# Optimization experiments

Measured on AMD Instinct MI355X. Metric: run time of the kernel, lower is better.

## Reference

```python
import jax, jax.numpy as jnp
import numpy as np

LN_EPS = 1e-5

def setup_inputs() -> dict:
    key = jax.random.key(0)
    k1, k2, k3 = jax.random.split(key, 3)
    L, B, D = 2048, 8, 1024
    x = jax.random.normal(k1, (L, B, D), dtype=jnp.float32)
    c = jnp.zeros((B, D), dtype=jnp.float32)
    W = jax.random.normal(k2, (D, 3 * D), dtype=jnp.float32) * 0.02
    # bias init from _init_bias: u-bias 0, f-bias 0.5, r-bias 0
    b = jnp.concatenate([jnp.zeros(D), jnp.full((D,), 0.5), jnp.zeros(D)]).astype(jnp.float32)
    gamma = jnp.ones((D,), dtype=jnp.float32)
    beta = jnp.zeros((D,), dtype=jnp.float32)
    return {"x": x, "c": c, "W": W, "b": b, "gamma": gamma, "beta": beta}

def reference(x, c, W, b, gamma, beta):
    # LayerNorm over last dim
    mu = jnp.mean(x, axis=-1, keepdims=True)
    var = jnp.mean(jnp.square(x - mu), axis=-1, keepdims=True)
    x_norm = (x - mu) * jax.lax.rsqrt(var + LN_EPS) * gamma + beta
    # Fused u/f/r projection: [L,B,3D]
    ufr = jnp.einsum('lbd,de->lbe', x_norm, W) + b
    u, f, r = jnp.split(ufr, 3, axis=-1)
    f_gate = jax.nn.sigmoid(f)
    r_gate = jax.nn.sigmoid(r)
    # Linear recurrence c_t = f_t * c_{t-1} + (1-f_t) * u_t via scan over time
    def step(c_prev, fu):
        f_t, u_t = fu
        c_t = f_t * c_prev + (1.0 - f_t) * u_t
        return c_t, c_t
    last_c, c_stack = jax.lax.scan(step, c, (f_gate, u))
    hs = r_gate * jnp.tanh(c_stack) + (1.0 - r_gate) * x_norm
    return x + hs, last_c
```

## Files before the change

kernel.cpp:

```cpp
#include <hip/hip_runtime.h>
#include <hip/hip_bf16.h>


typedef unsigned short u16;
typedef __bf16 bf16x8 __attribute__((ext_vector_type(8)));
typedef float f32x4 __attribute__((ext_vector_type(4)));

#define L_DIM 2048
#define B_DIM 8
#define D_DIM 1024
#define M_DIM (L_DIM * B_DIM)
#define K_DIM D_DIM
#define N_DIM (3 * D_DIM)
#define NCH 32
#define CLEN (L_DIM / NCH)
#define NT (K_DIM / 64)

#define LDS_A 0
#define LDS_B 65536
#define LDS_DUMMY 131072
#define LDS_TOTAL 147456

__device__ __forceinline__ float bf2f(u16 h) {
    unsigned int u = ((unsigned int)h) << 16;
    float f;
    __builtin_memcpy(&f, &u, 4);
    return f;
}

__device__ __forceinline__ u16 f2bf(float f) {
    unsigned int u;
    __builtin_memcpy(&u, &f, 4);
    u = u + 0x7fff + ((u >> 16) & 1);
    return (u16)(u >> 16);
}

__device__ __forceinline__ void async16(void* lds, const void* g) {
    __builtin_amdgcn_global_load_lds(
        (const __attribute__((address_space(1))) void*)g,
        (__attribute__((address_space(3))) void*)lds, 16, 0, 0);
}

__global__ __launch_bounds__(256) void ln_kernel(const float* __restrict__ x,
                                                 const float* __restrict__ gamma,
                                                 const float* __restrict__ beta,
                                                 u16* __restrict__ xn) {
    int row = blockIdx.x;
    int tid = threadIdx.x;
    const float4* xr = (const float4*)(x + (size_t)row * D_DIM);
    float4 v = xr[tid];
    float s = v.x + v.y + v.z + v.w;
    float q = v.x * v.x + v.y * v.y + v.z * v.z + v.w * v.w;
    #pragma unroll
    for (int off = 32; off; off >>= 1) {
        s += __shfl_down(s, off);
        q += __shfl_down(q, off);
    }
    __shared__ float ss[4], qq[4];
    int lane = tid & 63, wv = tid >> 6;
    if (lane == 0) { ss[wv] = s; qq[wv] = q; }
    __syncthreads();
    s = ss[0] + ss[1] + ss[2] + ss[3];
    q = qq[0] + qq[1] + qq[2] + qq[3];
    float mu = s * (1.0f / D_DIM);
    float var = q * (1.0f / D_DIM) - mu * mu;
    float rs = rsqrtf(var + 1e-5f);
    float4 g = ((const float4*)gamma)[tid];
    float4 bt = ((const float4*)beta)[tid];
    ushort4 o;
    o.x = f2bf((v.x - mu) * rs * g.x + bt.x);
    o.y = f2bf((v.y - mu) * rs * g.y + bt.y);
    o.z = f2bf((v.z - mu) * rs * g.z + bt.z);
    o.w = f2bf((v.w - mu) * rs * g.w + bt.w);
    ((ushort4*)(xn + (size_t)row * D_DIM))[tid] = o;
}

__global__ __launch_bounds__(256) void wt_kernel(const float* __restrict__ W,
                                                 u16* __restrict__ Wt) {
    __shared__ float t[64][65];
    int k0 = blockIdx.x * 64;
    int n0 = blockIdx.y * 64;
    int col = threadIdx.x & 63;
    int rg4 = threadIdx.x >> 6;
    #pragma unroll
    for (int j = 0; j < 16; ++j) {
        int r = rg4 * 16 + j;
        t[r][col] = W[(size_t)(k0 + r) * N_DIM + n0 + col];
    }
    __syncthreads();
    #pragma unroll
    for (int j = 0; j < 16; ++j) {
        int nr = rg4 * 16 + j;
        Wt[(size_t)(n0 + nr) * K_DIM + k0 + col] = f2bf(t[col][nr]);
    }
}

__device__ __forceinline__ void stage_half(const u16* __restrict__ gsrc, int base0,
                                           int t, int h, char* lds, int ldsOp,
                                           int tid, int wave) {
    int tc = (t < NT) ? t : 0;
    int k0 = tc * 64;
    char* dst0 = (t < NT) ? (lds + ldsOp + (t & 1) * 32768 + h * 16384)
                          : (lds + LDS_DUMMY);
    #pragma unroll
    for (int s = 0; s < 2; ++s) {
        int c = s * 512 + tid;
        int row = h * 128 + (c >> 3);
        int cc = (c & 7) ^ (row & 7);
        async16(dst0 + s * 8192 + wave * 1024,
                gsrc + (size_t)(base0 + row) * K_DIM + k0 + cc * 8);
    }
}

__global__ __launch_bounds__(512, 2) void gemm_kernel(const u16* __restrict__ A,
                                                      const u16* __restrict__ Bt,
                                                      const float* __restrict__ bias,
                                                      u16* __restrict__ uo,
                                                      u16* __restrict__ fo,
                                                      u16* __restrict__ ro) {
    extern __shared__ char lds[];
    const int tid = threadIdx.x;
    const int wave = tid >> 6, lane = tid & 63;
    const int lm = lane & 15, lg = lane >> 4;
    const int wm = wave >> 2, wn = wave & 3;
    const int m0 = blockIdx.x * 256;
    const int n0 = blockIdx.y * 256;

    f32x4 acc[8][4] = {};
    bf16x8 av[4][2], aw[4][2], bv[4][2];

#define LDA(dst, bb, mf0)                                                       \
    do { _Pragma("unroll")                                                      \
        for (int q = 0; q < 4; ++q) {                                           \
            int row_ = wm * 128 + ((mf0) + q) * 16 + lm;                        \
            const char* p_ = lds + LDS_A + (bb) * 32768 + row_ * 128;           \
            _Pragma("unroll")                                                   \
            for (int kk = 0; kk < 2; ++kk)                                      \
                dst[q][kk] = *(const bf16x8*)(p_ + ((((kk << 2) | lg) ^ (row_ & 7)) << 4)); \
        } } while (0)

#define LDB(bb, kk)                                                             \
    do { _Pragma("unroll")                                                      \
        for (int nf = 0; nf < 4; ++nf) {                                        \
            int row_ = wn * 64 + nf * 16 + lm;                                  \
            bv[nf][kk] = *(const bf16x8*)(lds + LDS_B + (bb) * 32768 + row_ * 128 \
                                          + ((((kk << 2) | lg) ^ (row_ & 7)) << 4)); \
        } } while (0)

#define MFMA16(r0, afr, kk)                                                     \
    do { _Pragma("unroll")                                                      \
        for (int q = 0; q < 4; ++q)                                             \
            _Pragma("unroll")                                                   \
            for (int nf = 0; nf < 4; ++nf)                                      \
                acc[(r0) + q][nf] = __builtin_amdgcn_mfma_f32_16x16x32_bf16(    \
                    afr[q][kk], bv[nf][kk], acc[(r0) + q][nf], 0, 0, 0);        \
    } while (0)

#define PH_SYNC()                                                               \
    do { __builtin_amdgcn_s_barrier();                                          \
         asm volatile("s_waitcnt lgkmcnt(0)");                                  \
         __builtin_amdgcn_sched_barrier(0); } while (0)

#define TILE_BODY(t, bb, last)                                                  \
    do {                                                                        \
                 \
        LDA(av, bb, 0);                                                         \
        LDB(bb, 0);                                                             \
        stage_half(A, m0, (t) + 1, 0, lds, LDS_A, tid, wave);                   \
        PH_SYNC();                                                              \
        __builtin_amdgcn_s_setprio(1);                                          \
        MFMA16(0, av, 0);                                                       \
        __builtin_amdgcn_s_setprio(0);                                          \
        __builtin_amdgcn_s_barrier();                                           \
                                     \
        LDB(bb, 1);                                                             \
        stage_half(A, m0, (t) + 1, 1, lds, LDS_A, tid, wave);                   \
        PH_SYNC();                                                              \
        __builtin_amdgcn_s_setprio(1);                                          \
        MFMA16(0, av, 1);                                                       \
        __builtin_amdgcn_s_setprio(0);                                          \
        __builtin_amdgcn_s_barrier();                                           \
                                   \
        LDA(aw, bb, 4);                                                         \
        stage_half(Bt, n0, (t) + 2, 0, lds, LDS_B, tid, wave);                  \
        PH_SYNC();                                                              \
        __builtin_amdgcn_s_setprio(1);                                          \
        MFMA16(4, aw, 0);                                                       \
        __builtin_amdgcn_s_setprio(0);                                          \
        __builtin_amdgcn_s_barrier();                                           \
                         \
        stage_half(Bt, n0, (t) + 2, 1, lds, LDS_B, tid, wave);                  \
        __builtin_amdgcn_s_barrier();                                           \
        __builtin_amdgcn_s_setprio(1);                                          \
        MFMA16(4, aw, 1);                                                       \
        __builtin_amdgcn_s_setprio(0);                                          \
        if (!(last)) asm volatile("s_waitcnt vmcnt(4)" ::: "memory");           \
        __builtin_amdgcn_s_barrier();                                           \
    } while (0)

    stage_half(A, m0, 0, 0, lds, LDS_A, tid, wave);
    stage_half(A, m0, 0, 1, lds, LDS_A, tid, wave);
    stage_half(Bt, n0, 0, 0, lds, LDS_B, tid, wave);
    stage_half(Bt, n0, 0, 1, lds, LDS_B, tid, wave);
    stage_half(Bt, n0, 1, 0, lds, LDS_B, tid, wave);
    stage_half(Bt, n0, 1, 1, lds, LDS_B, tid, wave);
    asm volatile("s_waitcnt vmcnt(4)" ::: "memory");
    __builtin_amdgcn_s_barrier();

    for (int t = 0; t < NT - 2; t += 2) {
        TILE_BODY(t, 0, 0);
        TILE_BODY(t + 1, 1, 0);
    }
    TILE_BODY(NT - 2, 0, 0);
    TILE_BODY(NT - 1, 1, 1);

    int seg = n0 >> 10;
    u16* outp = (seg == 0) ? uo : ((seg == 1) ? fo : ro);
    #pragma unroll
    for (int mf = 0; mf < 8; ++mf) {
        #pragma unroll
        for (int nf = 0; nf < 4; ++nf) {
            int col = n0 + wn * 64 + nf * 16 + lm;
            int cm = col & 1023;
            float bb2 = bias[col];
            #pragma unroll
            for (int j = 0; j < 4; ++j) {
                int row = m0 + wm * 128 + mf * 16 + lg * 4 + j;
                float val = acc[mf][nf][j] + bb2;
                if (seg != 0) val = 1.0f / (1.0f + __expf(-val));
                outp[(size_t)row * D_DIM + cm] = f2bf(val);
            }
        }
    }
#undef LDA
#undef LDB
#undef MFMA16
#undef PH_SYNC
#undef TILE_BODY
}

__global__ __launch_bounds__(256) void scan1_kernel(const u16* __restrict__ fg,
                                                    const u16* __restrict__ u,
                                                    float* __restrict__ Aa,
                                                    float* __restrict__ Ss) {
    int ch = blockIdx.x;
    int bd = (blockIdx.y * 256 + threadIdx.x) * 2;
    int b = bd >> 10, d = bd & 1023;
    float a0 = 1.0f, a1 = 1.0f, s0 = 0.0f, s1 = 0.0f;
    for (int t = ch * CLEN; t < ch * CLEN + CLEN; ++t) {
        size_t idx = ((size_t)(t * B_DIM + b) << 10) + d;
        ushort2 f2 = *(const ushort2*)(fg + idx);
        ushort2 u2 = *(const ushort2*)(u + idx);
        float f0 = bf2f(f2.x), f1 = bf2f(f2.y);
        float v0 = bf2f(u2.x), v1 = bf2f(u2.y);
        s0 = f0 * s0 + (1.0f - f0) * v0;
        s1 = f1 * s1 + (1.0f - f1) * v1;
        a0 *= f0;
        a1 *= f1;
    }
    int o = ch * 8192 + bd;
    *(float2*)(Aa + o) = make_float2(a0, a1);
    *(float2*)(Ss + o) = make_float2(s0, s1);
}

__global__ __launch_bounds__(256) void scan2_kernel(const float* __restrict__ Aa,
                                                    const float* __restrict__ Ss,
                                                    const float* __restrict__ c0,
                                                    float* __restrict__ cs,
                                                    float* __restrict__ lastc) {
    int bd = blockIdx.x * 256 + threadIdx.x;
    float c = c0[bd];
    #pragma unroll 4
    for (int ch = 0; ch < NCH; ++ch) {
        cs[ch * 8192 + bd] = c;
        c = Aa[ch * 8192 + bd] * c + Ss[ch * 8192 + bd];
    }
    lastc[bd] = c;
}

__global__ __launch_bounds__(256) void scan3_kernel(const float* __restrict__ cs,
                                                    const u16* __restrict__ fg,
                                                    const u16* __restrict__ u,
                                                    const u16* __restrict__ rg,
                                                    const u16* __restrict__ xn,
                                                    const float* __restrict__ x,
                                                    float* __restrict__ out) {
    int ch = blockIdx.x;
    int bd = (blockIdx.y * 256 + threadIdx.x) * 2;
    int b = bd >> 10, d = bd & 1023;
    float c0v = cs[ch * 8192 + bd];
    float c1v = cs[ch * 8192 + bd + 1];
    for (int t = ch * CLEN; t < ch * CLEN + CLEN; ++t) {
        size_t idx = ((size_t)(t * B_DIM + b) << 10) + d;
        ushort2 f2 = *(const ushort2*)(fg + idx);
        ushort2 u2 = *(const ushort2*)(u + idx);
        ushort2 r2 = *(const ushort2*)(rg + idx);
        ushort2 n2 = *(const ushort2*)(xn + idx);
        float2 x2 = *(const float2*)(x + idx);
        float f0 = bf2f(f2.x), f1 = bf2f(f2.y);
        float v0 = bf2f(u2.x), v1 = bf2f(u2.y);
        float r0 = bf2f(r2.x), r1 = bf2f(r2.y);
        float n0 = bf2f(n2.x), n1 = bf2f(n2.y);
        c0v = f0 * c0v + (1.0f - f0) * v0;
        c1v = f1 * c1v + (1.0f - f1) * v1;
        float h0 = r0 * tanhf(c0v) + (1.0f - r0) * n0;
        float h1 = r1 * tanhf(c1v) + (1.0f - r1) * n1;
        *(float2*)(out + idx) = make_float2(x2.x + h0, x2.y + h1);
    }
}

extern "C" void kernel_launch(void* const* d_in, const int* in_sizes, int n_in,
                              void* d_out, int out_size, void* d_ws, size_t ws_size,
                              hipStream_t stream) {
    const float* x     = (const float*)d_in[0];
    const float* c0    = (const float*)d_in[1];
    const float* W     = (const float*)d_in[2];
    const float* b     = (const float*)d_in[3];
    const float* gamma = (const float*)d_in[4];
    const float* beta  = (const float*)d_in[5];
    float* out = (float*)d_out;
    float* lastc = out + (size_t)M_DIM * D_DIM;

    char* w = (char*)d_ws;
    u16* xn = (u16*)w;  w += (size_t)M_DIM * D_DIM * 2;
    u16* Wt = (u16*)w;  w += (size_t)N_DIM * K_DIM * 2;
    u16* ug = (u16*)w;  w += (size_t)M_DIM * D_DIM * 2;
    u16* fg = (u16*)w;  w += (size_t)M_DIM * D_DIM * 2;
    u16* rg = (u16*)w;  w += (size_t)M_DIM * D_DIM * 2;
    float* Aa = (float*)w; w += (size_t)NCH * 8192 * 4;
    float* Ss = (float*)w; w += (size_t)NCH * 8192 * 4;
    float* cs = (float*)w; w += (size_t)NCH * 8192 * 4;

    hipFuncSetAttribute(reinterpret_cast<const void*>(gemm_kernel),
                        hipFuncAttributeMaxDynamicSharedMemorySize, LDS_TOTAL);

    ln_kernel<<<M_DIM, 256, 0, stream>>>(x, gamma, beta, xn);
    wt_kernel<<<dim3(K_DIM / 64, N_DIM / 64), 256, 0, stream>>>(W, Wt);
    gemm_kernel<<<dim3(M_DIM / 256, N_DIM / 256), 512, LDS_TOTAL, stream>>>(xn, Wt, b, ug, fg, rg);
    scan1_kernel<<<dim3(NCH, 16), 256, 0, stream>>>(fg, ug, Aa, Ss);
    scan2_kernel<<<32, 256, 0, stream>>>(Aa, Ss, c0, cs, lastc);
    scan3_kernel<<<dim3(NCH, 16), 256, 0, stream>>>(cs, fg, ug, rg, xn, x, out);
}
```

Measured before the change: 215.8 us.

## Make GEMM blocks persistent over three N tiles and recompute x_norm in scan

The GEMM grid shrinks from 64x12 blocks to 256 blocks. Each block keeps its A row-tile and loops over three consecutive 256-column N tiles, running a continuous prefetch pipeline across tile boundaries and writing each epilogue in turn. The aim is to cut launch/tail overhead and keep loads streaming between tiles, though the epilogue stores now sit in the loop. Separately, LayerNorm saves per-row mean and rstd, and the final scan kernel recomputes x_norm in fp32 from x instead of reading the bf16 xn buffer. This trades that read for a small per-row load plus some FMAs.

Result: slower. 233.2 us (+8.1%).

```diff
diff --git a/kernel.cpp b/kernel.cpp
--- a/kernel.cpp
+++ b/kernel.cpp
@@ -14,7 +14,9 @@
 #define N_DIM (3 * D_DIM)
 #define NCH 32
 #define CLEN (L_DIM / NCH)
-#define NT (K_DIM / 64)
+#define NT 16
+#define NREP 3
+#define GTOT (NT * NREP)
 
 #define LDS_A 0
 #define LDS_B 65536
@@ -44,7 +46,8 @@
 __global__ __launch_bounds__(256) void ln_kernel(const float* __restrict__ x,
                                                  const float* __restrict__ gamma,
                                                  const float* __restrict__ beta,
-                                                 u16* __restrict__ xn) {
+                                                 u16* __restrict__ xn,
+                                                 float2* __restrict__ mrs) {
     int row = blockIdx.x;
     int tid = threadIdx.x;
     const float4* xr = (const float4*)(x + (size_t)row * D_DIM);
@@ -65,6 +68,7 @@
     float mu = s * (1.0f / D_DIM);
     float var = q * (1.0f / D_DIM) - mu * mu;
     float rs = rsqrtf(var + 1e-5f);
+    if (tid == 0) mrs[row] = make_float2(mu, rs);
     float4 g = ((const float4*)gamma)[tid];
     float4 bt = ((const float4*)beta)[tid];
     ushort4 o;
@@ -95,23 +99,6 @@
     }
 }
 
-__device__ __forceinline__ void stage_half(const u16* __restrict__ gsrc, int base0,
-                                           int t, int h, char* lds, int ldsOp,
-                                           int tid, int wave) {
-    int tc = (t < NT) ? t : 0;
-    int k0 = tc * 64;
-    char* dst0 = (t < NT) ? (lds + ldsOp + (t & 1) * 32768 + h * 16384)
-                          : (lds + LDS_DUMMY);
-    #pragma unroll
-    for (int s = 0; s < 2; ++s) {
-        int c = s * 512 + tid;
-        int row = h * 128 + (c >> 3);
-        int cc = (c & 7) ^ (row & 7);
-        async16(dst0 + s * 8192 + wave * 1024,
-                gsrc + (size_t)(base0 + row) * K_DIM + k0 + cc * 8);
-    }
-}
-
 __global__ __launch_bounds__(512, 2) void gemm_kernel(const u16* __restrict__ A,
                                                       const u16* __restrict__ Bt,
                                                       const float* __restrict__ bias,
@@ -123,20 +110,48 @@
     const int wave = tid >> 6, lane = tid & 63;
     const int lm = lane & 15, lg = lane >> 4;
     const int wm = wave >> 2, wn = wave & 3;
-    const int m0 = blockIdx.x * 256;
-    const int n0 = blockIdx.y * 256;
-
-    f32x4 acc[8][4] = {};
-    bf16x8 av[4][2], aw[4][2], bv[4][2];
-
-#define LDA(dst, bb, mf0)                                                       \
+    const int bid = blockIdx.x;
+    const int m0 = (bid & 63) * 256;
+    const int n0base = (bid >> 6) * 768;
+
+    const int c0 = tid, c1 = 512 + tid;
+    const int r0 = c0 >> 3, cc0 = (c0 & 7) ^ (r0 & 7);
+    const int r1 = c1 >> 3, cc1 = (c1 & 7) ^ (r1 & 7);
+    const char* gA0 = (const char*)A + ((size_t)(m0 + r0) * K_DIM + cc0 * 8) * 2;
+    const char* gA1 = (const char*)A + ((size_t)(m0 + r1) * K_DIM + cc1 * 8) * 2;
+    const int boB0 = (r0 * K_DIM + cc0 * 8) * 2;
+    const int boB1 = (r1 * K_DIM + cc1 * 8) * 2;
+    char* dstBase = lds + wave * 1024;
+
+    f32x4 acc[8][4];
+    bf16x8 av[4][2], bv[4][2];
+
+    auto stageA = [&](int g1, int h) {
+        char* dst = (g1 < GTOT) ? (dstBase + (g1 & 1) * 32768 + h * 16384)
+                                : (lds + LDS_DUMMY + wave * 1024);
+        int kb = ((g1 & 15) << 7) + (h << 18);
+        async16(dst,        gA0 + kb);
+        async16(dst + 8192, gA1 + kb);
+    };
+    auto stageB = [&](int g2, int h) {
+        char* dst = (g2 < GTOT) ? (dstBase + LDS_B + (g2 & 1) * 32768 + h * 16384)
+                                : (lds + LDS_DUMMY + wave * 1024);
+        int gc = (g2 < GTOT) ? g2 : 0;
+        const char* src = (const char*)Bt
+            + (size_t)(n0base + (gc >> 4) * 256) * (K_DIM * 2)
+            + ((gc & 15) << 7) + (h << 18);
+        async16(dst,        src + boB0);
+        async16(dst + 8192, src + boB1);
+    };
+
+#define LDA(bb, mf0)                                                            \
     do { _Pragma("unroll")                                                      \
         for (int q = 0; q < 4; ++q) {                                           \
             int row_ = wm * 128 + ((mf0) + q) * 16 + lm;                        \
             const char* p_ = lds + LDS_A + (bb) * 32768 + row_ * 128;           \
             _Pragma("unroll")                                                   \
             for (int kk = 0; kk < 2; ++kk)                                      \
-                dst[q][kk] = *(const bf16x8*)(p_ + ((((kk << 2) | lg) ^ (row_ & 7)) << 4)); \
+                av[q][kk] = *(const bf16x8*)(p_ + ((((kk << 2) | lg) ^ (lm & 7)) << 4)); \
         } } while (0)
 
 #define LDB(bb, kk)                                                             \
@@ -144,16 +159,16 @@
         for (int nf = 0; nf < 4; ++nf) {                                        \
             int row_ = wn * 64 + nf * 16 + lm;                                  \
             bv[nf][kk] = *(const bf16x8*)(lds + LDS_B + (bb) * 32768 + row_ * 128 \
-                                          + ((((kk << 2) | lg) ^ (row_ & 7)) << 4)); \
+                                          + ((((kk << 2) | lg) ^ (lm & 7)) << 4)); \
         } } while (0)
 
-#define MFMA16(r0, afr, kk)                                                     \
+#define MFMA16(r0q, kk)                                                         \
     do { _Pragma("unroll")                                                      \
         for (int q = 0; q < 4; ++q)                                             \
             _Pragma("unroll")                                                   \
             for (int nf = 0; nf < 4; ++nf)                                      \
-                acc[(r0) + q][nf] = __builtin_amdgcn_mfma_f32_16x16x32_bf16(    \
-                    afr[q][kk], bv[nf][kk], acc[(r0) + q][nf], 0, 0, 0);        \
+                acc[(r0q) + q][nf] = __builtin_amdgcn_mfma_f32_16x16x32_bf16(   \
+                    av[q][kk], bv[nf][kk], acc[(r0q) + q][nf], 0, 0, 0);        \
     } while (0)
 
 #define PH_SYNC()                                                               \
@@ -161,74 +176,68 @@
          asm volatile("s_waitcnt lgkmcnt(0)");                                  \
          __builtin_amdgcn_sched_barrier(0); } while (0)
 
-#define TILE_BODY(t, bb, last)                                                  \
+#define TILE_BODY(g, bb)                                                        \
     do {                                                                        \
-                 \
-        LDA(av, bb, 0);                                                         \
+        LDA(bb, 0);                                                             \
         LDB(bb, 0);                                                             \
-        stage_half(A, m0, (t) + 1, 0, lds, LDS_A, tid, wave);                   \
+        stageA((g) + 1, 0);                                                     \
         PH_SYNC();                                                              \
-        __builtin_amdgcn_s_setprio(1);                                          \
-        MFMA16(0, av, 0);                                                       \
+        __builtin_amdgcn_s_setprio(1);  MFMA16(0, 0);                           \
+        __builtin_amdgcn_s_setprio(0);  __builtin_amdgcn_s_barrier();           \
+        LDB(bb, 1);                                                             \
+        stageA((g) + 1, 1);                                                     \
+        PH_SYNC();                                                              \
+        __builtin_amdgcn_s_setprio(1);  MFMA16(0, 1);                           \
+        __builtin_amdgcn_s_setprio(0);  __builtin_amdgcn_s_barrier();           \
+        LDA(bb, 4);                                                             \
+        stageB((g) + 2, 0);                                                     \
+        PH_SYNC();                                                              \
+        __builtin_amdgcn_s_setprio(1);  MFMA16(4, 0);                           \
+        __builtin_amdgcn_s_setprio(0);  __builtin_amdgcn_s_barrier();           \
+        stageB((g) + 2, 1);                                                     \
+        __builtin_amdgcn_s_barrier();                                           \
+        __builtin_amdgcn_s_setprio(1);  MFMA16(4, 1);                           \
         __builtin_amdgcn_s_setprio(0);                                          \
-        __builtin_amdgcn_s_barrier();                                           \
-                                     \
-        LDB(bb, 1);                                                             \
-        stage_half(A, m0, (t) + 1, 1, lds, LDS_A, tid, wave);                   \
-        PH_SYNC();                                                              \
-        __builtin_amdgcn_s_setprio(1);                                          \
-        MFMA16(0, av, 1);                                                       \
-        __builtin_amdgcn_s_setprio(0);                                          \
-        __builtin_amdgcn_s_barrier();                                           \
-                                   \
-        LDA(aw, bb, 4);                                                         \
-        stage_half(Bt, n0, (t) + 2, 0, lds, LDS_B, tid, wave);                  \
-        PH_SYNC();                                                              \
-        __builtin_amdgcn_s_setprio(1);                                          \
-        MFMA16(4, aw, 0);                                                       \
-        __builtin_amdgcn_s_setprio(0);                                          \
-        __builtin_amdgcn_s_barrier();                                           \
-                         \
-        stage_half(Bt, n0, (t) + 2, 1, lds, LDS_B, tid, wave);                  \
-        __builtin_amdgcn_s_barrier();                                           \
-        __builtin_amdgcn_s_setprio(1);                                          \
-        MFMA16(4, aw, 1);                                                       \
-        __builtin_amdgcn_s_setprio(0);                                          \
-        if (!(last)) asm volatile("s_waitcnt vmcnt(4)" ::: "memory");           \
+        asm volatile("s_waitcnt vmcnt(4)" ::: "memory");                        \
         __builtin_amdgcn_s_barrier();                                           \
     } while (0)
 
-    stage_half(A, m0, 0, 0, lds, LDS_A, tid, wave);
-    stage_half(A, m0, 0, 1, lds, LDS_A, tid, wave);
-    stage_half(Bt, n0, 0, 0, lds, LDS_B, tid, wave);
-    stage_half(Bt, n0, 0, 1, lds, LDS_B, tid, wave);
-    stage_half(Bt, n0, 1, 0, lds, LDS_B, tid, wave);
-    stage_half(Bt, n0, 1, 1, lds, LDS_B, tid, wave);
+    stageA(0, 0); stageA(0, 1);
+    stageB(0, 0); stageB(0, 1);
+    stageB(1, 0); stageB(1, 1);
     asm volatile("s_waitcnt vmcnt(4)" ::: "memory");
     __builtin_amdgcn_s_barrier();
 
-    for (int t = 0; t < NT - 2; t += 2) {
-        TILE_BODY(t, 0, 0);
-        TILE_BODY(t + 1, 1, 0);
-    }
-    TILE_BODY(NT - 2, 0, 0);
-    TILE_BODY(NT - 1, 1, 1);
-
-    int seg = n0 >> 10;
-    u16* outp = (seg == 0) ? uo : ((seg == 1) ? fo : ro);
-    #pragma unroll
-    for (int mf = 0; mf < 8; ++mf) {
+    #pragma unroll 1
+    for (int rep = 0; rep < NREP; ++rep) {
+        #pragma unroll
+        for (int i = 0; i < 8; ++i)
+            #pragma unroll
+            for (int j = 0; j < 4; ++j)
+                acc[i][j] = (f32x4){0.f, 0.f, 0.f, 0.f};
+        const int gbase = rep * NT;
+        #pragma unroll 1
+        for (int t = 0; t < NT; t += 2) {
+            TILE_BODY(gbase + t, 0);
+            TILE_BODY(gbase + t + 1, 1);
+        }
+        int n0 = n0base + rep * 256;
+        int seg = n0 >> 10;
+        u16* outp = (seg == 0) ? uo : ((seg == 1) ? fo : ro);
         #pragma unroll
         for (int nf = 0; nf < 4; ++nf) {
             int col = n0 + wn * 64 + nf * 16 + lm;
             int cm = col & 1023;
             float bb2 = bias[col];
             #pragma unroll
-            for (int j = 0; j < 4; ++j) {
-                int row = m0 + wm * 128 + mf * 16 + lg * 4 + j;
-                float val = acc[mf][nf][j] + bb2;
-                if (seg != 0) val = 1.0f / (1.0f + __expf(-val));
-                outp[(size_t)row * D_DIM + cm] = f2bf(val);
+            for (int mf = 0; mf < 8; ++mf) {
+                #pragma unroll
+                for (int j = 0; j < 4; ++j) {
+                    int row = m0 + wm * 128 + mf * 16 + lg * 4 + j;
+                    float val = acc[mf][nf][j] + bb2;
+                    if (seg != 0) val = 1.0f / (1.0f + __expf(-val));
+                    outp[(size_t)row * D_DIM + cm] = f2bf(val);
+                }
             }
         }
     }
@@ -282,12 +291,16 @@
                                                     const u16* __restrict__ fg,
                                                     const u16* __restrict__ u,
                                                     const u16* __restrict__ rg,
-                                                    const u16* __restrict__ xn,
+                                                    const float2* __restrict__ mrs,
+                                                    const float* __restrict__ gamma,
+                                                    const float* __restrict__ beta,
                                                     const float* __restrict__ x,
                                                     float* __restrict__ out) {
     int ch = blockIdx.x;
     int bd = (blockIdx.y * 256 + threadIdx.x) * 2;
     int b = bd >> 10, d = bd & 1023;
+    float2 gm = *(const float2*)(gamma + d);
+    float2 bt = *(const float2*)(beta + d);
     float c0v = cs[ch * 8192 + bd];
     float c1v = cs[ch * 8192 + bd + 1];
     for (int t = ch * CLEN; t < ch * CLEN + CLEN; ++t) {
@@ -295,12 +308,13 @@
         ushort2 f2 = *(const ushort2*)(fg + idx);
         ushort2 u2 = *(const ushort2*)(u + idx);
         ushort2 r2 = *(const ushort2*)(rg + idx);
-        ushort2 n2 = *(const ushort2*)(xn + idx);
         float2 x2 = *(const float2*)(x + idx);
+        float2 mr = mrs[t * B_DIM + b];
         float f0 = bf2f(f2.x), f1 = bf2f(f2.y);
         float v0 = bf2f(u2.x), v1 = bf2f(u2.y);
         float r0 = bf2f(r2.x), r1 = bf2f(r2.y);
-        float n0 = bf2f(n2.x), n1 = bf2f(n2.y);
+        float n0 = (x2.x - mr.x) * mr.y * gm.x + bt.x;
+        float n1 = (x2.y - mr.x) * mr.y * gm.y + bt.y;
         c0v = f0 * c0v + (1.0f - f0) * v0;
         c1v = f1 * c1v + (1.0f - f1) * v1;
         float h0 = r0 * tanhf(c0v) + (1.0f - r0) * n0;
@@ -330,14 +344,15 @@
     float* Aa = (float*)w; w += (size_t)NCH * 8192 * 4;
     float* Ss = (float*)w; w += (size_t)NCH * 8192 * 4;
     float* cs = (float*)w; w += (size_t)NCH * 8192 * 4;
+    float2* mrs = (float2*)w; w += (size_t)M_DIM * 8;
 
     hipFuncSetAttribute(reinterpret_cast<const void*>(gemm_kernel),
                         hipFuncAttributeMaxDynamicSharedMemorySize, LDS_TOTAL);
 
-    ln_kernel<<<M_DIM, 256, 0, stream>>>(x, gamma, beta, xn);
+    ln_kernel<<<M_DIM, 256, 0, stream>>>(x, gamma, beta, xn, mrs);
     wt_kernel<<<dim3(K_DIM / 64, N_DIM / 64), 256, 0, stream>>>(W, Wt);
-    gemm_kernel<<<dim3(M_DIM / 256, N_DIM / 256), 512, LDS_TOTAL, stream>>>(xn, Wt, b, ug, fg, rg);
+    gemm_kernel<<<256, 512, LDS_TOTAL, stream>>>(xn, Wt, b, ug, fg, rg);
     scan1_kernel<<<dim3(NCH, 16), 256, 0, stream>>>(fg, ug, Aa, Ss);
     scan2_kernel<<<32, 256, 0, stream>>>(Aa, Ss, c0, cs, lastc);
-    scan3_kernel<<<dim3(NCH, 16), 256, 0, stream>>>(cs, fg, ug, rg, xn, x, out);
-}
+    scan3_kernel<<<dim3(NCH, 16), 256, 0, stream>>>(cs, fg, ug, rg, mrs, gamma, beta, x, out);
+}
```
